# Kernel optimization log

Hardware: AMD Instinct MI355X
Metric: run time of the kernel (lower is better)

The kernel has to match this reference:

```python
import jax, jax.numpy as jnp
import numpy as np

N_CH = 256          # EEG channels = graph nodes
T = 100000          # timesteps
CNN_OUT = 32
GRU_H = 64
GNN_H = 32
N_CLS = 2
THRESH = 0.7


def _conv1d(x, w, b, stride, pad):
    # x: [N, C_in, L], w: [C_out, C_in, K]
    y = jax.lax.conv_general_dilated(
        x, w, window_strides=(stride,), padding=[(pad, pad)],
        dimension_numbers=("NCH", "OIH", "NCH"))
    return y + b[None, :, None]


def _gru_last_hidden(xs, wih, whh, bih, bhh):
    # xs: [S, N, in], returns final hidden [N, H] (PyTorch GRU equations)
    H = whh.shape[1]
    h0 = jnp.zeros((xs.shape[1], H), xs.dtype)

    def step(h, x):
        gi = x @ wih.T + bih          # [N, 3H]
        gh = h @ whh.T + bhh
        i_r, i_z, i_n = jnp.split(gi, 3, axis=-1)
        h_r, h_z, h_n = jnp.split(gh, 3, axis=-1)
        r = jax.nn.sigmoid(i_r + h_r)
        z = jax.nn.sigmoid(i_z + h_z)
        n = jnp.tanh(i_n + r * h_n)
        h = (1.0 - z) * n + z * h
        return h, None

    hT, _ = jax.lax.scan(step, h0, xs)
    return hT


def _pairwise_corrcoef(x):
    x = x - x.mean(axis=1, keepdims=True)
    x = x / (x.std(axis=1, keepdims=True, ddof=1) + 1e-6)  # torch std is unbiased
    return (x @ x.T) / x.shape[1]


def _gcn(x, A_hat, w, b):
    # PyG GCNConv: A_hat @ (x @ W^T) + b  (sym-normalized adj w/ self-loops)
    return A_hat @ (x @ w.T) + b


def setup_inputs() -> dict:
    key = jax.random.key(0)
    ks = jax.random.split(key, 24)
    r = lambda i, shape, s: (jax.random.normal(ks[i], shape, jnp.float32) * s)
    d = {
        "data": r(0, (N_CH, T), 1.0),
        "conv1_w": r(1, (8, 1, 11), 0.3), "conv1_b": r(2, (8,), 0.1),
        "conv2_w": r(3, (16, 8, 7), 0.1), "conv2_b": r(4, (16,), 0.1),
        "conv3_w": r(5, (CNN_OUT, 16, 5), 0.1), "conv3_b": r(6, (CNN_OUT,), 0.1),
        "gru_wih_f": r(7, (3 * GRU_H, CNN_OUT), 0.1), "gru_whh_f": r(8, (3 * GRU_H, GRU_H), 0.1),
        "gru_bih_f": r(9, (3 * GRU_H,), 0.05), "gru_bhh_f": r(10, (3 * GRU_H,), 0.05),
        "gru_wih_b": r(11, (3 * GRU_H, CNN_OUT), 0.1), "gru_whh_b": r(12, (3 * GRU_H, GRU_H), 0.1),
        "gru_bih_b": r(13, (3 * GRU_H,), 0.05), "gru_bhh_b": r(14, (3 * GRU_H,), 0.05),
        "gcn1_w": r(15, (GNN_H, 2 * GRU_H), 0.1), "gcn1_b": r(16, (GNN_H,), 0.05),
        "gcn2_w": r(17, (GNN_H, GNN_H), 0.15), "gcn2_b": r(18, (GNN_H,), 0.05),
        "cls_w": r(19, (N_CLS, GNN_H), 0.15), "cls_b": r(20, (N_CLS,), 0.05),
    }
    return d


def reference(data, conv1_w, conv1_b, conv2_w, conv2_b, conv3_w, conv3_b,
              gru_wih_f, gru_whh_f, gru_bih_f, gru_bhh_f,
              gru_wih_b, gru_whh_b, gru_bih_b, gru_bhh_b,
              gcn1_w, gcn1_b, gcn2_w, gcn2_b, cls_w, cls_b):
    x = data[:, None, :]                                 # [N, 1, T]
    x = jax.nn.relu(_conv1d(x, conv1_w, conv1_b, 5, 5))  # [N, 8, 20000]
    x = jax.nn.relu(_conv1d(x, conv2_w, conv2_b, 5, 3))  # [N, 16, 4000]
    x = jax.nn.relu(_conv1d(x, conv3_w, conv3_b, 5, 2))  # [N, 32, 800]
    xs = jnp.transpose(x, (2, 0, 1))                     # [S=800, N, 32]

    h_f = _gru_last_hidden(xs, gru_wih_f, gru_whh_f, gru_bih_f, gru_bhh_f)
    h_b = _gru_last_hidden(xs[::-1], gru_wih_b, gru_whh_b, gru_bih_b, gru_bhh_b)
    # torch h_n.permute(1,0,2).reshape(N,-1) -> concat [fwd, bwd]
    h_n = jnp.concatenate([h_f, h_b], axis=-1)           # [N, 128]

    corr = _pairwise_corrcoef(h_n)                       # [N, N]
    # dense adjacency = thresholded |corr|; diagonal is ~1 so self-loops present
    # (matches PyG add_remaining_self_loops: already there). Always nonempty.
    A = (jnp.abs(corr) > THRESH).astype(h_n.dtype)
    deg = A.sum(axis=1)
    dinv = jax.lax.rsqrt(jnp.maximum(deg, 1e-12))
    A_hat = A * dinv[:, None] * dinv[None, :]            # D^-1/2 A D^-1/2

    h = jax.nn.relu(_gcn(h_n, A_hat, gcn1_w, gcn1_b))
    h = jax.nn.relu(_gcn(h, A_hat, gcn2_w, gcn2_b))
    graph_emb = h.mean(axis=0, keepdims=True)            # [1, GNN_H]
    return graph_emb @ cls_w.T + cls_b                   # [1, N_CLS]
```

## Files before the change

kernel.cpp:

```cpp
#include <hip/hip_runtime.h>
#include <math.h>

#define N_CH 256
#define T_IN 100000
#define L1O 20000
#define L2O 4000
#define L3O 800
#define C1 8
#define C2 16
#define C3 32

#define TILE3 25
#define NY2   125
#define NY1   627
#define ND    3141

__device__ __forceinline__ float sigm(float x) {
    x = fminf(fmaxf(x, -30.0f), 30.0f);
    return 1.0f / (1.0f + __expf(-x));
}
__device__ __forceinline__ float tanhfast(float x) {
    x = fminf(fmaxf(x, -15.0f), 15.0f);
    float e = __expf(-2.0f * x);
    return (1.0f - e) / (1.0f + e);
}
__device__ __forceinline__ float dot4(float4 a, float4 b) {
    return a.x * b.x + a.y * b.y + a.z * b.z + a.w * b.w;
}

__global__ __launch_bounds__(256) void k_conv(
    const float* __restrict__ data,
    const float* __restrict__ w1, const float* __restrict__ b1,
    const float* __restrict__ w2, const float* __restrict__ b2,
    const float* __restrict__ w3, const float* __restrict__ b3,
    float* __restrict__ x3)
{
    __shared__ __align__(16) float sd[ND];
    __shared__ __align__(16) float sy1[NY1][C1];
    __shared__ __align__(16) float sy2[NY2][C2];
    __shared__ __align__(16) float sw1[C1 * 11];
    __shared__ float sb1[C1];
    __shared__ __align__(16) float sw2[C2 * C1 * 7];
    __shared__ float sb2[C2];
    __shared__ __align__(16) float sw3[C3 * C2 * 5];
    __shared__ float sb3[C3];

    const int tid = threadIdx.x;
    const int tb  = blockIdx.x;
    const int ch  = blockIdx.y;
    const int t0    = tb * TILE3;
    const int dbase = 3125 * tb - 70;
    const int ubase = 625 * tb - 13;
    const int sbase = 125 * tb - 2;

    for (int e = tid; e < C1 * 11;    e += 256) sw1[e] = w1[e];
    for (int e = tid; e < C1;         e += 256) sb1[e] = b1[e];
    for (int e = tid; e < C2 * C1 * 7; e += 256) sw2[e] = w2[e];
    for (int e = tid; e < C2;         e += 256) sb2[e] = b2[e];
    for (int e = tid; e < C3 * C2 * 5; e += 256) sw3[e] = w3[e];
    for (int e = tid; e < C3;         e += 256) sb3[e] = b3[e];

    const float* dch = data + (size_t)ch * T_IN;
    for (int e = tid; e < ND; e += 256) {
        int g = dbase + e;
        sd[e] = (g >= 0 && g < T_IN) ? dch[g] : 0.0f;
    }
    __syncthreads();

    {
        const int c = tid & 7;
        float wr[11];
        #pragma unroll
        for (int k = 0; k < 11; ++k) wr[k] = sw1[c * 11 + k];
        const float bb = sb1[c];
        for (int u = tid >> 3; u < NY1; u += 32) {
            int ug = ubase + u;
            float acc = bb;
            #pragma unroll
            for (int k = 0; k < 11; ++k) acc += wr[k] * sd[5 * u + k];
            sy1[u][c] = (ug >= 0 && ug < L1O) ? fmaxf(acc, 0.0f) : 0.0f;
        }
    }
    __syncthreads();

    {
        const int c = tid & 15;
        float wr[56];
        #pragma unroll
        for (int q = 0; q < 14; ++q)
            ((float4*)wr)[q] = ((const float4*)(sw2 + c * 56))[q];
        const float bb = sb2[c];
        for (int s = tid >> 4; s < NY2; s += 16) {
            int sg = sbase + s;
            float acc = bb;
            #pragma unroll
            for (int k = 0; k < 7; ++k) {
                const float4* y4 = (const float4*)&sy1[5 * s + k][0];
                float4 ya = y4[0], yb = y4[1];
                acc += wr[0*7+k]*ya.x + wr[1*7+k]*ya.y + wr[2*7+k]*ya.z + wr[3*7+k]*ya.w
                     + wr[4*7+k]*yb.x + wr[5*7+k]*yb.y + wr[6*7+k]*yb.z + wr[7*7+k]*yb.w;
            }
            sy2[s][c] = (sg >= 0 && sg < L2O) ? fmaxf(acc, 0.0f) : 0.0f;
        }
    }
    __syncthreads();

    {
        const int o = tid & 31;
        float wr[80];
        #pragma unroll
        for (int q = 0; q < 20; ++q)
            ((float4*)wr)[q] = ((const float4*)(sw3 + o * 80))[q];
        const float bb = sb3[o];
        for (int tl = tid >> 5; tl < TILE3; tl += 8) {
            float acc = bb;
            #pragma unroll
            for (int k = 0; k < 5; ++k) {
                const float4* y4 = (const float4*)&sy2[5 * tl + k][0];
                float4 za = y4[0], zb = y4[1], zc = y4[2], zd = y4[3];
                acc += wr[0*5+k]*za.x  + wr[1*5+k]*za.y  + wr[2*5+k]*za.z  + wr[3*5+k]*za.w
                     + wr[4*5+k]*zb.x  + wr[5*5+k]*zb.y  + wr[6*5+k]*zb.z  + wr[7*5+k]*zb.w
                     + wr[8*5+k]*zc.x  + wr[9*5+k]*zc.y  + wr[10*5+k]*zc.z + wr[11*5+k]*zc.w
                     + wr[12*5+k]*zd.x + wr[13*5+k]*zd.y + wr[14*5+k]*zd.z + wr[15*5+k]*zd.w;
            }
            x3[((size_t)ch * L3O + (t0 + tl)) * C3 + o] = fmaxf(acc, 0.0f);
        }
    }
}

__global__ __launch_bounds__(192) void k_gi(
    const float* __restrict__ x3,
    const float* __restrict__ wih_f, const float* __restrict__ bih_f,
    const float* __restrict__ wih_b, const float* __restrict__ bih_b,
    float* __restrict__ Gi, int c0, int CH)
{
    const int row = threadIdx.x;
    const int dirch = blockIdx.x;
    const int dir = dirch >> 8, ch = dirch & 255;
    const int tt0 = blockIdx.y * 25;
    const float* wih = dir ? wih_b : wih_f;
    const float* bih = dir ? bih_b : bih_f;
    __shared__ __align__(16) float sx[25][32];

    for (int e = row; e < 25 * 32; e += 192) {
        int tt = e >> 5, k = e & 31;
        int step = c0 + tt0 + tt;
        int tm = dir ? (L3O - 1 - step) : step;
        sx[tt][k] = x3[((size_t)ch * L3O + tm) * 32 + k];
    }
    float4 w[8];
    const float4* w4 = (const float4*)(wih + row * 32);
    #pragma unroll
    for (int q = 0; q < 8; ++q) w[q] = w4[q];
    const float bb = bih[row];
    __syncthreads();

    float* gout = Gi + ((size_t)dirch * CH + tt0) * 192 + row;
    for (int tt = 0; tt < 25; ++tt) {
        const float4* x4 = (const float4*)&sx[tt][0];
        float a0 = 0, a1 = 0, a2 = 0, a3 = 0;
        #pragma unroll
        for (int q = 0; q < 8; q += 4) {
            a0 += dot4(w[q],     x4[q]);
            a1 += dot4(w[q + 1], x4[q + 1]);
            a2 += dot4(w[q + 2], x4[q + 2]);
            a3 += dot4(w[q + 3], x4[q + 3]);
        }
        gout[tt * 192] = bb + ((a0 + a1) + (a2 + a3));
    }
}

__global__ __launch_bounds__(64, 1) void k_gru2(
    const float* __restrict__ Gi,
    const float* __restrict__ whh_f, const float* __restrict__ bhh_f,
    const float* __restrict__ whh_b, const float* __restrict__ bhh_b,
    float* __restrict__ hN, int t0, int tlen, int CH)
{
    const int lane = threadIdx.x;
    const int ch = blockIdx.x, dir = blockIdx.y;
    const int dirch = dir * 256 + ch;
    const float* whh = dir ? whh_b : whh_f;
    const float* bhh = dir ? bhh_b : bhh_f;
    __shared__ __align__(16) float sh[64];

    float4 whr[16], whz[16], whn[16];
    const float4* whh4 = (const float4*)whh;
    #pragma unroll
    for (int j = 0; j < 16; ++j) {
        whr[j] = whh4[(0   + lane) * 16 + j];
        whz[j] = whh4[(64  + lane) * 16 + j];
        whn[j] = whh4[(128 + lane) * 16 + j];
    }
    const float bhr = bhh[lane], bhz = bhh[64 + lane], bhn = bhh[128 + lane];

    float h = (t0 == 0) ? 0.0f : hN[ch * 128 + dir * 64 + lane];
    sh[lane] = h;
    __syncthreads();

    const float* gp = Gi + (size_t)dirch * CH * 192;
    float gr = gp[lane], gz = gp[64 + lane], gn = gp[128 + lane];
    for (int tl = 0; tl < tlen; ++tl) {
        const float* gpn = gp + 192;
        float grn = 0.f, gzn = 0.f, gnn = 0.f;
        if (tl + 1 < tlen) { grn = gpn[lane]; gzn = gpn[64 + lane]; gnn = gpn[128 + lane]; }

        float hr0=0,hr1=0,hr2=0,hr3=0, hz0=0,hz1=0,hz2=0,hz3=0, hn0=0,hn1=0,hn2=0,hn3=0;
        const float4* sh4 = (const float4*)sh;
        #pragma unroll
        for (int j = 0; j < 16; j += 4) {
            float4 a = sh4[j], b = sh4[j+1], c = sh4[j+2], d = sh4[j+3];
            hr0 += dot4(whr[j],   a); hr1 += dot4(whr[j+1], b);
            hr2 += dot4(whr[j+2], c); hr3 += dot4(whr[j+3], d);
            hz0 += dot4(whz[j],   a); hz1 += dot4(whz[j+1], b);
            hz2 += dot4(whz[j+2], c); hz3 += dot4(whz[j+3], d);
            hn0 += dot4(whn[j],   a); hn1 += dot4(whn[j+1], b);
            hn2 += dot4(whn[j+2], c); hn3 += dot4(whn[j+3], d);
        }
        float r = sigm(gr + bhr + ((hr0 + hr1) + (hr2 + hr3)));
        float z = sigm(gz + bhz + ((hz0 + hz1) + (hz2 + hz3)));
        float hnv = ((hn0 + hn1) + (hn2 + hn3)) + bhn;
        float n = tanhfast(gn + r * hnv);
        h = (1.0f - z) * n + z * h;
        __syncthreads();
        sh[lane] = h;
        __syncthreads();
        gr = grn; gz = gzn; gn = gnn; gp = gpn;
    }
    hN[ch * 128 + dir * 64 + lane] = h;
}

#define CHUNK 100
__global__ __launch_bounds__(64) void k_gru(
    const float* __restrict__ x3,
    const float* __restrict__ wih_f, const float* __restrict__ whh_f,
    const float* __restrict__ bih_f, const float* __restrict__ bhh_f,
    const float* __restrict__ wih_b, const float* __restrict__ whh_b,
    const float* __restrict__ bih_b, const float* __restrict__ bhh_b,
    float* __restrict__ hN)
{
    const int lane = threadIdx.x;
    const int ch   = blockIdx.x;
    const int dir  = blockIdx.y;
    const float* wih = dir ? wih_b : wih_f;
    const float* whh = dir ? whh_b : whh_f;
    const float* bih = dir ? bih_b : bih_f;
    const float* bhh = dir ? bhh_b : bhh_f;

    __shared__ __align__(16) float sh[64];
    __shared__ __align__(16) float sx[CHUNK * 32];

    float4 wir[8], wiz[8], win[8];
    const float4* wih4 = (const float4*)wih;
    #pragma unroll
    for (int k = 0; k < 8; ++k) {
        wir[k] = wih4[(0   + lane) * 8 + k];
        wiz[k] = wih4[(64  + lane) * 8 + k];
        win[k] = wih4[(128 + lane) * 8 + k];
    }
    float4 whr[16], whz[16], whn[16];
    const float4* whh4 = (const float4*)whh;
    #pragma unroll
    for (int j = 0; j < 16; ++j) {
        whr[j] = whh4[(0   + lane) * 16 + j];
        whz[j] = whh4[(64  + lane) * 16 + j];
        whn[j] = whh4[(128 + lane) * 16 + j];
    }
    const float bir = bih[lane], biz = bih[64 + lane], bin_ = bih[128 + lane];
    const float bhr = bhh[lane], bhz = bhh[64 + lane], bhn  = bhh[128 + lane];

    float h = 0.0f;
    sh[lane] = 0.0f;
    __syncthreads();

    const float* xch = x3 + (size_t)ch * L3O * 32;
    for (int c0 = 0; c0 < L3O; c0 += CHUNK) {
        for (int e = lane; e < CHUNK * 32; e += 64) {
            int tt = e >> 5, k = e & 31;
            int sidx = c0 + tt;
            int t = dir ? (L3O - 1 - sidx) : sidx;
            sx[e] = xch[t * 32 + k];
        }
        __syncthreads();
        for (int tl = 0; tl < CHUNK; ++tl) {
            const float4* xv4 = (const float4*)(sx + tl * 32);
            float gr = 0.f, gz = 0.f, gn = 0.f;
            #pragma unroll
            for (int k = 0; k < 8; ++k) {
                float4 x4 = xv4[k];
                gr += dot4(wir[k], x4); gz += dot4(wiz[k], x4); gn += dot4(win[k], x4);
            }
            float hr = 0.f, hz = 0.f, hn = 0.f;
            const float4* sh4 = (const float4*)sh;
            #pragma unroll
            for (int j = 0; j < 16; ++j) {
                float4 h4 = sh4[j];
                hr += dot4(whr[j], h4); hz += dot4(whz[j], h4); hn += dot4(whn[j], h4);
            }
            float r = sigm(gr + bir + hr + bhr);
            float z = sigm(gz + biz + hz + bhz);
            float n = tanhfast(gn + bin_ + r * (hn + bhn));
            h = (1.0f - z) * n + z * h;
            __syncthreads();
            sh[lane] = h;
            __syncthreads();
        }
    }
    hN[ch * 128 + dir * 64 + lane] = h;
}

__global__ __launch_bounds__(128) void k_norm(
    const float* __restrict__ hN, const float* __restrict__ gcn1_w,
    float* __restrict__ Xn, float* __restrict__ XnT, float* __restrict__ hw1)
{
    const int i = blockIdx.x, tid = threadIdx.x;
    __shared__ float red[128];
    __shared__ float row[128];
    float v = hN[i * 128 + tid];
    row[tid] = v;
    red[tid] = v;
    __syncthreads();
    for (int s = 64; s > 0; s >>= 1) { if (tid < s) red[tid] += red[tid + s]; __syncthreads(); }
    float mean = red[0] / 128.0f;
    __syncthreads();
    float d = v - mean;
    red[tid] = d * d;
    __syncthreads();
    for (int s = 64; s > 0; s >>= 1) { if (tid < s) red[tid] += red[tid + s]; __syncthreads(); }
    float sd = sqrtf(red[0] / 127.0f);
    float xn = d / (sd + 1e-6f);
    Xn[i * 128 + tid] = xn;
    XnT[tid * 256 + i] = xn;
    if (tid < 32) {
        float acc = 0.f;
        for (int k = 0; k < 128; ++k) acc += row[k] * gcn1_w[tid * 128 + k];
        hw1[i * 32 + tid] = acc;
    }
}

__global__ __launch_bounds__(256) void k_corr(
    const float* __restrict__ Xn, const float* __restrict__ XnT,
    float* __restrict__ A, float* __restrict__ deg)
{
    const int i = blockIdx.x, tid = threadIdx.x;
    __shared__ float xi[128];
    __shared__ float red[256];
    if (tid < 128) xi[tid] = Xn[i * 128 + tid];
    __syncthreads();
    float c = 0.f;
    for (int k = 0; k < 128; ++k) c += xi[k] * XnT[k * 256 + tid];
    c *= (1.0f / 128.0f);
    float a = (fabsf(c) > 0.7f) ? 1.0f : 0.0f;
    A[i * 256 + tid] = a;
    red[tid] = a;
    __syncthreads();
    for (int s = 128; s > 0; s >>= 1) { if (tid < s) red[tid] += red[tid + s]; __syncthreads(); }
    if (tid == 0) deg[i] = red[0];
}

__global__ __launch_bounds__(256) void k_gcn(
    const float* __restrict__ A, const float* __restrict__ deg,
    const float* __restrict__ hw, const float* __restrict__ bias,
    const float* __restrict__ wNext,
    float* __restrict__ hOut, float* __restrict__ hwNext)
{
    const int i = blockIdx.x, tid = threadIdx.x;
    const int f = tid & 31, grp = tid >> 5;
    __shared__ float aj[256];
    __shared__ float red[8][32];
    __shared__ float hrow[32];
    float dj = rsqrtf(fmaxf(deg[tid], 1e-12f));
    aj[tid] = A[i * 256 + tid] * dj;
    __syncthreads();
    float p = 0.f;
    for (int j = grp * 32; j < grp * 32 + 32; ++j) p += aj[j] * hw[j * 32 + f];
    red[grp][f] = p;
    __syncthreads();
    if (grp == 0) {
        float s = 0.f;
        #pragma unroll
        for (int g = 0; g < 8; ++g) s += red[g][f];
        float di = rsqrtf(fmaxf(deg[i], 1e-12f));
        float o = fmaxf(bias[f] + di * s, 0.0f);
        hOut[i * 32 + f] = o;
        hrow[f] = o;
    }
    __syncthreads();
    if (wNext != nullptr && grp == 0) {
        float acc = 0.f;
        #pragma unroll
        for (int k = 0; k < 32; ++k) acc += hrow[k] * wNext[f * 32 + k];
        hwNext[i * 32 + f] = acc;
    }
}

__global__ __launch_bounds__(64) void k_head(
    const float* __restrict__ h2, const float* __restrict__ cls_w,
    const float* __restrict__ cls_b, float* __restrict__ out)
{
    const int tid = threadIdx.x;
    __shared__ float mean[32];
    if (tid < 32) {
        float s = 0.f;
        for (int i = 0; i < 256; ++i) s += h2[i * 32 + tid];
        mean[tid] = s * (1.0f / 256.0f);
    }
    __syncthreads();
    if (tid < 2) {
        float s = cls_b[tid];
        #pragma unroll
        for (int fe = 0; fe < 32; ++fe) s += mean[fe] * cls_w[tid * 32 + fe];
        out[tid] = s;
    }
}

extern "C" void kernel_launch(void* const* d_in, const int* in_sizes, int n_in,
                              void* d_out, int out_size, void* d_ws, size_t ws_size,
                              hipStream_t stream) {
    const float* data    = (const float*)d_in[0];
    const float* conv1_w = (const float*)d_in[1];
    const float* conv1_b = (const float*)d_in[2];
    const float* conv2_w = (const float*)d_in[3];
    const float* conv2_b = (const float*)d_in[4];
    const float* conv3_w = (const float*)d_in[5];
    const float* conv3_b = (const float*)d_in[6];
    const float* wih_f   = (const float*)d_in[7];
    const float* whh_f   = (const float*)d_in[8];
    const float* bih_f   = (const float*)d_in[9];
    const float* bhh_f   = (const float*)d_in[10];
    const float* wih_b   = (const float*)d_in[11];
    const float* whh_b   = (const float*)d_in[12];
    const float* bih_b   = (const float*)d_in[13];
    const float* bhh_b   = (const float*)d_in[14];
    const float* gcn1_w  = (const float*)d_in[15];
    const float* gcn1_b  = (const float*)d_in[16];
    const float* gcn2_w  = (const float*)d_in[17];
    const float* gcn2_b  = (const float*)d_in[18];
    const float* cls_w   = (const float*)d_in[19];
    const float* cls_b   = (const float*)d_in[20];

    float* ws  = (float*)d_ws;
    float* x3  = ws;
    float* hN  = x3 + 6553600;
    float* Xn  = hN + 32768;
    float* XnT = Xn + 32768;
    float* A   = XnT + 32768;
    float* deg = A + 65536;
    float* hw1 = deg + 256;
    float* h1  = hw1 + 8192;
    float* hw2 = h1 + 8192;
    float* h2  = hw2 + 8192;
    float* Gi  = h2 + 8192;

    const size_t BASE = 6726272;
    const size_t avail = ws_size / 4;
    int CH = 0;
    if      (avail >= BASE + (size_t)512 * 800 * 192) CH = 800;
    else if (avail >= BASE + (size_t)512 * 100 * 192) CH = 100;
    else if (avail >= BASE + (size_t)512 *  50 * 192) CH = 50;
    else if (avail >= BASE + (size_t)512 *  25 * 192) CH = 25;

    k_conv<<<dim3(32, 256), 256, 0, stream>>>(data, conv1_w, conv1_b, conv2_w, conv2_b,
                                              conv3_w, conv3_b, x3);
    if (CH) {
        for (int c0 = 0; c0 < L3O; c0 += CH) {
            k_gi<<<dim3(512, CH / 25), 192, 0, stream>>>(x3, wih_f, bih_f, wih_b, bih_b,
                                                         Gi, c0, CH);
            k_gru2<<<dim3(256, 2), 64, 0, stream>>>(Gi, whh_f, bhh_f, whh_b, bhh_b,
                                                    hN, c0, CH, CH);
        }
    } else {
        k_gru<<<dim3(256, 2), 64, 0, stream>>>(x3, wih_f, whh_f, bih_f, bhh_f,
                                               wih_b, whh_b, bih_b, bhh_b, hN);
    }
    k_norm<<<256, 128, 0, stream>>>(hN, gcn1_w, Xn, XnT, hw1);
    k_corr<<<256, 256, 0, stream>>>(Xn, XnT, A, deg);
    k_gcn<<<256, 256, 0, stream>>>(A, deg, hw1, gcn1_b, gcn2_w, h1, hw2);
    k_gcn<<<256, 256, 0, stream>>>(A, deg, hw2, gcn2_b, nullptr, h2, nullptr);
    k_head<<<1, 64, 0, stream>>>(h2, cls_w, cls_b, (float*)d_out);
}
```

Baseline: 1.220 ms.

## Broadcast GRU hidden state via readlane instead of LDS with barriers

The recurrent GRU step kernel no longer writes the hidden state to shared memory and synchronises twice per timestep. Each lane's hidden value is broadcast across the wavefront with readlane and consumed by scalar FMAs against weights held in registers. The Gi input prefetch is also deepened to two steps ahead. This removes LDS round-trips and barriers from the serial 800-step critical path, but readlane broadcasts go through scalar registers and can add per-step latency.

```diff
diff --git a/kernel.cpp b/kernel.cpp
--- a/kernel.cpp
+++ b/kernel.cpp
@@ -15,6 +15,8 @@
 #define NY1   627
 #define ND    3141
 
+#define KEEP1(x) asm volatile("" : "+v"(x))
+
 __device__ __forceinline__ float sigm(float x) {
     x = fminf(fmaxf(x, -30.0f), 30.0f);
     return 1.0f / (1.0f + __expf(-x));
@@ -26,6 +28,9 @@
 }
 __device__ __forceinline__ float dot4(float4 a, float4 b) {
     return a.x * b.x + a.y * b.y + a.z * b.z + a.w * b.w;
+}
+__device__ __forceinline__ float bcast(float v, int lane) {
+    return __int_as_float(__builtin_amdgcn_readlane(__float_as_int(v), lane));
 }
 
 __global__ __launch_bounds__(256) void k_conv(
@@ -170,7 +175,7 @@
     }
 }
 
-__global__ __launch_bounds__(64, 1) void k_gru2(
+__global__ __launch_bounds__(64, 1) void k_gru3(
     const float* __restrict__ Gi,
     const float* __restrict__ whh_f, const float* __restrict__ bhh_f,
     const float* __restrict__ whh_b, const float* __restrict__ bhh_b,
@@ -181,50 +186,55 @@
     const int dirch = dir * 256 + ch;
     const float* whh = dir ? whh_b : whh_f;
     const float* bhh = dir ? bhh_b : bhh_f;
-    __shared__ __align__(16) float sh[64];
-
-    float4 whr[16], whz[16], whn[16];
+
+    float wr[64], wz[64], wn[64];
     const float4* whh4 = (const float4*)whh;
     #pragma unroll
-    for (int j = 0; j < 16; ++j) {
-        whr[j] = whh4[(0   + lane) * 16 + j];
-        whz[j] = whh4[(64  + lane) * 16 + j];
-        whn[j] = whh4[(128 + lane) * 16 + j];
-    }
+    for (int q = 0; q < 16; ++q) {
+        float4 a = whh4[(0   + lane) * 16 + q];
+        float4 b = whh4[(64  + lane) * 16 + q];
+        float4 c = whh4[(128 + lane) * 16 + q];
+        wr[4*q] = a.x; wr[4*q+1] = a.y; wr[4*q+2] = a.z; wr[4*q+3] = a.w;
+        wz[4*q] = b.x; wz[4*q+1] = b.y; wz[4*q+2] = b.z; wz[4*q+3] = b.w;
+        wn[4*q] = c.x; wn[4*q+1] = c.y; wn[4*q+2] = c.z; wn[4*q+3] = c.w;
+    }
+    #pragma unroll
+    for (int j = 0; j < 64; ++j) { KEEP1(wr[j]); KEEP1(wz[j]); KEEP1(wn[j]); }
+
     const float bhr = bhh[lane], bhz = bhh[64 + lane], bhn = bhh[128 + lane];
 
     float h = (t0 == 0) ? 0.0f : hN[ch * 128 + dir * 64 + lane];
-    sh[lane] = h;
-    __syncthreads();
 
     const float* gp = Gi + (size_t)dirch * CH * 192;
-    float gr = gp[lane], gz = gp[64 + lane], gn = gp[128 + lane];
+    float g0r = gp[lane], g0z = gp[64 + lane], g0n = gp[128 + lane];
+    gp += 192;
+    float g1r = gp[lane], g1z = gp[64 + lane], g1n = gp[128 + lane];
+    gp += 192;
+
     for (int tl = 0; tl < tlen; ++tl) {
-        const float* gpn = gp + 192;
-        float grn = 0.f, gzn = 0.f, gnn = 0.f;
-        if (tl + 1 < tlen) { grn = gpn[lane]; gzn = gpn[64 + lane]; gnn = gpn[128 + lane]; }
-
-        float hr0=0,hr1=0,hr2=0,hr3=0, hz0=0,hz1=0,hz2=0,hz3=0, hn0=0,hn1=0,hn2=0,hn3=0;
-        const float4* sh4 = (const float4*)sh;
-        #pragma unroll
-        for (int j = 0; j < 16; j += 4) {
-            float4 a = sh4[j], b = sh4[j+1], c = sh4[j+2], d = sh4[j+3];
-            hr0 += dot4(whr[j],   a); hr1 += dot4(whr[j+1], b);
-            hr2 += dot4(whr[j+2], c); hr3 += dot4(whr[j+3], d);
-            hz0 += dot4(whz[j],   a); hz1 += dot4(whz[j+1], b);
-            hz2 += dot4(whz[j+2], c); hz3 += dot4(whz[j+3], d);
-            hn0 += dot4(whn[j],   a); hn1 += dot4(whn[j+1], b);
-            hn2 += dot4(whn[j+2], c); hn3 += dot4(whn[j+3], d);
-        }
-        float r = sigm(gr + bhr + ((hr0 + hr1) + (hr2 + hr3)));
-        float z = sigm(gz + bhz + ((hz0 + hz1) + (hz2 + hz3)));
-        float hnv = ((hn0 + hn1) + (hn2 + hn3)) + bhn;
-        float n = tanhfast(gn + r * hnv);
+        float g2r = 0.f, g2z = 0.f, g2n = 0.f;
+        if (tl + 2 < tlen) { g2r = gp[lane]; g2z = gp[64 + lane]; g2n = gp[128 + lane]; }
+        gp += 192;
+
+        float ar0 = 0.f, ar1 = 0.f, az0 = 0.f, az1 = 0.f, an0 = 0.f, an1 = 0.f;
+        #pragma unroll
+        for (int j = 0; j < 64; j += 2) {
+            float hj0 = bcast(h, j);
+            float hj1 = bcast(h, j + 1);
+            ar0 = fmaf(wr[j],     hj0, ar0);
+            az0 = fmaf(wz[j],     hj0, az0);
+            an0 = fmaf(wn[j],     hj0, an0);
+            ar1 = fmaf(wr[j + 1], hj1, ar1);
+            az1 = fmaf(wz[j + 1], hj1, az1);
+            an1 = fmaf(wn[j + 1], hj1, an1);
+        }
+        float r = sigm(g0r + bhr + (ar0 + ar1));
+        float z = sigm(g0z + bhz + (az0 + az1));
+        float n = tanhfast(g0n + r * ((an0 + an1) + bhn));
         h = (1.0f - z) * n + z * h;
-        __syncthreads();
-        sh[lane] = h;
-        __syncthreads();
-        gr = grn; gz = gzn; gn = gnn; gp = gpn;
+
+        g0r = g1r; g0z = g1z; g0n = g1n;
+        g1r = g2r; g1z = g2z; g1n = g2n;
     }
     hN[ch * 128 + dir * 64 + lane] = h;
 }
@@ -465,7 +475,7 @@
         for (int c0 = 0; c0 < L3O; c0 += CH) {
             k_gi<<<dim3(512, CH / 25), 192, 0, stream>>>(x3, wih_f, bih_f, wih_b, bih_b,
                                                          Gi, c0, CH);
-            k_gru2<<<dim3(256, 2), 64, 0, stream>>>(Gi, whh_f, bhh_f, whh_b, bhh_b,
+            k_gru3<<<dim3(256, 2), 64, 0, stream>>>(Gi, whh_f, bhh_f, whh_b, bhh_b,
                                                     hN, c0, CH, CH);
         }
     } else {
```

Result: faster. 977.7 us (-19.8%).
